# Performance work log

Measured on AMD Instinct MI355X. Metric: run time of the kernel, lower is better.

## Reference

```python
import jax, jax.numpy as jnp
import numpy as np

DIM = 256; HEADS = 8; HD = DIM // HEADS; WIN = 3; LOCAL = WIN * WIN
SR = 8; SHARED = 4; ROUTED = 2
B = 4; RES = 64; TBL = 4096
EPS = 1.1920929e-07  # torch.finfo(float32).eps


def _l2(x):
    return x / jnp.clip(jnp.linalg.norm(x, axis=-1, keepdims=True), EPS)


def _forward(x, relative_coords_table, q_w, q_b, kv_w, kv_b, temperature,
             query_embedding, rpb_local, learnable_tokens, learnable_bias,
             cpb1_w, cpb1_b, cpb2_w, cpb2_b, sr_w, sr_b, norm_g, norm_b,
             wg_w, wg0_w, wg1_w, proj_w, proj_b, relative_pos_index, H, W):
    B_, N, C = x.shape
    pH, pW = H // SR, W // SR
    PL = pH * pW
    _x = x.reshape(B_ * N, C)

    # ---- MoE head routing: top-k gating over routed heads ----
    gates = jax.nn.softmax(_x @ wg_w.T, axis=1)                 # (BN, n_routed)
    _, idx = jax.lax.top_k(gates, ROUTED)
    mask = jax.nn.one_hot(idx, gates.shape[1], dtype=gates.dtype).sum(axis=1)
    rg = gates * mask
    rg = rg / jnp.clip(jnp.sum(rg, axis=1, keepdims=True), EPS)
    routed_gates = rg.reshape(B_, N, -1) * ROUTED

    # ---- seq-length-scale buffer: log(local valid-window count + pool_len) ----
    r = WIN // 2
    ch = np.minimum(np.arange(H) + r, H - 1) - np.maximum(np.arange(H) - r, 0) + 1
    cw = np.minimum(np.arange(W) + r, W - 1) - np.maximum(np.arange(W) - r, 0) + 1
    sls = jnp.asarray(np.log(np.outer(ch, cw).reshape(-1, 1).astype(np.float32) + PL))

    # ---- queries ----
    q = (x @ q_w.T + q_b).reshape(B_, N, HEADS, HD).transpose(0, 2, 1, 3)
    q_norm = _l2(q)                                             # (B,h,N,d)
    q_scaled = (q_norm + query_embedding) * jax.nn.softplus(temperature) * sls

    # ---- local branch: unfold normalized k and v over 3x3 windows (zero pad) ----
    kv = x @ kv_w.T + kv_b                                      # (B,N,2C)
    k_loc = _l2(kv[..., :C].reshape(B_, N, HEADS, HD)).reshape(B_, N, C)
    kvl = jnp.concatenate([k_loc, kv[..., C:]], -1).transpose(0, 2, 1).reshape(B_, 2 * C, H, W)
    kvp = jnp.pad(kvl, ((0, 0), (0, 0), (r, r), (r, r)))
    patches = jnp.stack([kvp[:, :, i:i + H, j:j + W] for i in range(WIN) for j in range(WIN)], axis=2)
    patches = patches.reshape(B_, 2 * HEADS, HD, LOCAL, N).transpose(0, 1, 4, 2, 3)  # (B,2h,N,d,L)
    k_local, v_local = patches[:, :HEADS], patches[:, HEADS:]

    attn_local = jnp.einsum('bhnd,bhndl->bhnl', q_scaled, k_local) + rpb_local[:, None, :]

    # ---- pooled global branch ----
    x_ = x.transpose(0, 2, 1).reshape(B_, C, H, W)
    x_ = jnp.einsum('oc,bchw->bohw', sr_w, x_) + sr_b[None, :, None, None]  # 1x1 conv
    x_ = jax.nn.gelu(x_, approximate=False)
    x_ = x_.reshape(B_, C, pH, SR, pW, SR).mean((3, 5)).reshape(B_, C, PL).transpose(0, 2, 1)
    mu = x_.mean(-1, keepdims=True)
    var = ((x_ - mu) ** 2).mean(-1, keepdims=True)
    x_ = (x_ - mu) / jnp.sqrt(var + 1e-5) * norm_g + norm_b
    kvp2 = (x_ @ kv_w.T + kv_b).reshape(B_, PL, 2 * HEADS, HD).transpose(0, 2, 1, 3)
    k_pool, v_pool = kvp2[:, :HEADS], kvp2[:, HEADS:]

    cpb = jax.nn.relu(relative_coords_table @ cpb1_w.T + cpb1_b) @ cpb2_w.T + cpb2_b  # (T,h)
    pool_bias = cpb.T[:, relative_pos_index.reshape(-1)].reshape(HEADS, N, PL)
    attn_pool = jnp.einsum('bhnd,bhpd->bhnp', q_scaled, _l2(k_pool)) + pool_bias

    # ---- joint softmax over local + pooled keys ----
    attn = jax.nn.softmax(jnp.concatenate([attn_local, attn_pool], axis=-1), axis=-1)
    a_loc, a_pool = attn[..., :LOCAL], attn[..., LOCAL:]
    a_loc = jnp.einsum('bhnd,hdl->bhnl', q_norm, learnable_tokens) + learnable_bias + a_loc
    x_local = jnp.einsum('bhnl,bhndl->bhnd', a_loc, v_local)
    x_pool = jnp.einsum('bhnp,bhpd->bhnd', a_pool, v_pool)
    out = (x_local + x_pool).transpose(0, 2, 1, 3)              # (B,N,h,d)

    # ---- combine shared + routed head gates ----
    shared_gates = jax.nn.softmax(_x @ wg1_w.T, axis=1).reshape(B_, N, SHARED) * SHARED
    w0 = jax.nn.softmax(_x @ wg0_w.T, axis=1).reshape(B_, N, 2) * 2
    masked = jnp.concatenate([w0[..., 0:1] * shared_gates, w0[..., 1:2] * routed_gates], axis=-1)
    out = (masked[..., None] * out).reshape(B_, N, C)
    return out @ proj_w.T + proj_b


def setup_inputs() -> dict:
    key = jax.random.key(0)
    ks = jax.random.split(key, 20)
    H = W = RES
    N = H * W
    C = DIM
    PL = (H // SR) * (W // SR)

    def nrm(i, shape, s=0.02):
        return jax.random.normal(ks[i], shape, dtype=jnp.float32) * s

    return {
        'x': jax.random.normal(ks[0], (B, N, C), dtype=jnp.float32),
        'relative_coords_table': jax.random.normal(ks[1], (TBL, 2), dtype=jnp.float32),
        'q_w': nrm(3, (C, C)), 'q_b': jnp.zeros((C,), jnp.float32),
        'kv_w': nrm(4, (2 * C, C)), 'kv_b': jnp.zeros((2 * C,), jnp.float32),
        'temperature': jnp.full((HEADS, 1, 1), float(np.log(np.exp(1 / 0.24) - 1)), jnp.float32),
        'query_embedding': nrm(5, (HEADS, 1, HD)),
        'rpb_local': nrm(6, (HEADS, LOCAL), 0.0004),
        'learnable_tokens': nrm(7, (HEADS, HD, LOCAL)),
        'learnable_bias': jnp.zeros((HEADS, 1, LOCAL), jnp.float32),
        'cpb1_w': nrm(8, (512, 2)), 'cpb1_b': jnp.zeros((512,), jnp.float32),
        'cpb2_w': nrm(9, (HEADS, 512)), 'cpb2_b': jnp.zeros((HEADS,), jnp.float32),
        'sr_w': nrm(10, (C, C)), 'sr_b': jnp.zeros((C,), jnp.float32),
        'norm_g': jnp.ones((C,), jnp.float32), 'norm_b': jnp.zeros((C,), jnp.float32),
        'wg_w': nrm(11, (HEADS - SHARED, C)),
        'wg0_w': nrm(12, (2, C)),
        'wg1_w': nrm(13, (SHARED, C)),
        'proj_w': nrm(14, (C, C)), 'proj_b': jnp.zeros((C,), jnp.float32),
        'relative_pos_index': jax.random.randint(ks[2], (N, PL), 0, TBL, dtype=jnp.int32),
        'H': H, 'W': W,
    }


def reference(x, relative_coords_table, q_w, q_b, kv_w, kv_b, temperature,
              query_embedding, rpb_local, learnable_tokens, learnable_bias,
              cpb1_w, cpb1_b, cpb2_w, cpb2_b, sr_w, sr_b, norm_g, norm_b,
              wg_w, wg0_w, wg1_w, proj_w, proj_b, relative_pos_index, H, W):
    return _forward(x, relative_coords_table, q_w, q_b, kv_w, kv_b, temperature,
                    query_embedding, rpb_local, learnable_tokens, learnable_bias,
                    cpb1_w, cpb1_b, cpb2_w, cpb2_b, sr_w, sr_b, norm_g, norm_b,
                    wg_w, wg0_w, wg1_w, proj_w, proj_b, relative_pos_index, H, W)
```

## Files before the change

### kernel.cpp

```cpp
#include <hip/hip_runtime.h>
#include <math.h>

#define EPSF 1.1920929e-07f

typedef __attribute__((ext_vector_type(8))) short short8;
typedef __attribute__((ext_vector_type(4))) float f32x4;

static __device__ __forceinline__ unsigned short f2bf(float f) {
    unsigned int u = __float_as_uint(f);
    return (unsigned short)((u + 0x7FFFu + ((u >> 16) & 1u)) >> 16);
}
static __device__ __forceinline__ float bf2f(unsigned short u) {
    return __uint_as_float((unsigned int)u << 16);
}

__global__ __launch_bounds__(256) void prep_kernel(
    const float* __restrict__ x,
    const float* __restrict__ wg,  const float* __restrict__ wg0,
    const float* __restrict__ wg1,
    const float* __restrict__ q_w, const float* __restrict__ kv_w,
    const float* __restrict__ sr_w, const float* __restrict__ pw,
    const float* __restrict__ tbl,
    const float* __restrict__ c1w, const float* __restrict__ c1b,
    const float* __restrict__ c2w, const float* __restrict__ c2b,
    unsigned short* __restrict__ xbf, float* __restrict__ gate,
    unsigned short* __restrict__ wcat, unsigned short* __restrict__ pwbf,
    float* __restrict__ kv_wT, float* __restrict__ cpb)
{
    __shared__ float shpad[512];
    const int blk = blockIdx.x;
    const int t   = threadIdx.x;
    if (blk < 4096) {
        const int j = t & 63;
        const int row = (blk << 2) + (t >> 6);
        float4 v = *(const float4*)(x + (size_t)row*256 + j*4);
        ushort4 o;
        o.x = f2bf(v.x); o.y = f2bf(v.y); o.z = f2bf(v.z); o.w = f2bf(v.w);
        *(ushort4*)(xbf + (size_t)row*256 + j*4) = o;
        float d[10];
#pragma unroll
        for (int f = 0; f < 10; ++f) {
            const float* wf = (f < 4) ? (wg + f*256) : (f < 6) ? (wg0 + (f-4)*256)
                                                               : (wg1 + (f-6)*256);
            float4 wv = *(const float4*)(wf + j*4);
            float s = v.x*wv.x + v.y*wv.y + v.z*wv.z + v.w*wv.w;
            s += __shfl_xor(s, 32); s += __shfl_xor(s, 16); s += __shfl_xor(s, 8);
            s += __shfl_xor(s, 4);  s += __shfl_xor(s, 2);  s += __shfl_xor(s, 1);
            d[f] = s;
        }
        if (j == 0) {
            float e[4];
            float m = fmaxf(fmaxf(d[0],d[1]), fmaxf(d[2],d[3]));
            float ssum = 0.f;
            for (int i = 0; i < 4; ++i) { e[i] = expf(d[i]-m); ssum += e[i]; }
            for (int i = 0; i < 4; ++i) e[i] /= ssum;
            int i1 = 0;
            for (int i = 1; i < 4; ++i) if (e[i] > e[i1]) i1 = i;
            int i2 = -1;
            for (int i = 0; i < 4; ++i) if (i != i1 && (i2 < 0 || e[i] > e[i2])) i2 = i;
            float rs = fmaxf(e[i1] + e[i2], EPSF);
            float rg[4] = {0.f,0.f,0.f,0.f};
            rg[i1] = e[i1] / rs * 2.f;
            rg[i2] = e[i2] / rs * 2.f;
            float sh[4];
            float m1 = fmaxf(fmaxf(d[6],d[7]), fmaxf(d[8],d[9]));
            float s1 = 0.f;
            for (int i = 0; i < 4; ++i) { sh[i] = expf(d[6+i]-m1); s1 += sh[i]; }
            float mm = fmaxf(d[4], d[5]);
            float e0 = expf(d[4]-mm), e1 = expf(d[5]-mm);
            float w00 = e0/(e0+e1)*2.f, w01 = e1/(e0+e1)*2.f;
            float* gr = gate + ((size_t)row << 3);
            for (int i = 0; i < 4; ++i) gr[i]   = w00 * (sh[i]/s1*4.f);
            for (int i = 0; i < 4; ++i) gr[4+i] = w01 * rg[i];
        }
    } else if (blk < 4416) {
        const int e = ((blk - 4096)*256 + t)*4;
        if (e < 262144) {
            int n = e >> 8, k = e & 255;
            const float* src = (n < 256) ? (q_w + n*256) :
                               (n < 768) ? (kv_w + (n-256)*256) : (sr_w + (n-768)*256);
            float4 v = *(const float4*)(src + k);
            ushort4 o;
            o.x = f2bf(v.x); o.y = f2bf(v.y); o.z = f2bf(v.z); o.w = f2bf(v.w);
            *(ushort4*)(wcat + e) = o;
        } else {
            int e2 = e - 262144;
            float4 v = *(const float4*)(pw + e2);
            ushort4 o;
            o.x = f2bf(v.x); o.y = f2bf(v.y); o.z = f2bf(v.z); o.w = f2bf(v.w);
            *(ushort4*)(pwbf + e2) = o;
        }
    } else if (blk < 4544) {
        const int e = ((blk - 4416)*256 + t)*4;
        int o = e >> 8, k = e & 255;
        float4 v = *(const float4*)(kv_w + e);
        kv_wT[(k+0)*512 + o] = v.x;
        kv_wT[(k+1)*512 + o] = v.y;
        kv_wT[(k+2)*512 + o] = v.z;
        kv_wT[(k+3)*512 + o] = v.w;
    } else {
        const int r = blk - 4544;
        const float c0 = tbl[(size_t)r*2], c1 = tbl[(size_t)r*2+1];
        for (int i = t; i < 512; i += 256)
            shpad[i] = fmaxf(c0*c1w[i*2] + c1*c1w[i*2+1] + c1b[i], 0.f);
        __syncthreads();
        const int hh = t >> 5, dd = t & 31;
        float s = 0.f;
        for (int i = dd; i < 512; i += 32) s += shpad[i] * c2w[hh*512+i];
        for (int off = 16; off; off >>= 1) s += __shfl_xor(s, off, 32);
        if (dd == 0) cpb[((size_t)r << 3) + hh] = s + c2b[hh];
    }
}

__global__ __launch_bounds__(256) void gemm_mfma(
    const unsigned short* __restrict__ A,
    const unsigned short* __restrict__ W,
    const float* __restrict__ B0, const float* __restrict__ B1,
    const float* __restrict__ B2,
    int r1, int r2, int mode,
    float* __restrict__ C, int ldc,
    unsigned short* __restrict__ qkv,
    const float* __restrict__ temp, const float* __restrict__ qe)
{
    __shared__ __attribute__((aligned(16))) unsigned short Bt[64*264];
    const int m0 = blockIdx.y << 6;
    const int n0 = blockIdx.x << 6;
    const int t  = threadIdx.x;
    const int w  = t >> 6;
    const int col16 = t & 15;
    const int quad  = (t & 63) >> 4;

    const float* Bp; int noff;
    if (n0 < r1)      { Bp = B0; noff = 0;  }
    else if (n0 < r2) { Bp = B1; noff = r1; }
    else              { Bp = B2; noff = r2; }

    short8 afr[8];
    {
        const unsigned short* ap = A + (size_t)(m0 + w*16 + col16)*256 + quad*8;
#pragma unroll
        for (int kk = 0; kk < 8; ++kk)
            afr[kk] = *(const short8*)(ap + kk*32);
    }
#pragma unroll
    for (int j = 0; j < 8; ++j) {
        int ci = j*256 + t;
        int r = ci >> 5, c = ci & 31;
        uint4 bv = *(const uint4*)(W + (size_t)(n0 + r)*256 + c*8);
        *(uint4*)(Bt + r*264 + c*8) = bv;
    }
    __syncthreads();

    f32x4 acc[4];
#pragma unroll
    for (int ct = 0; ct < 4; ++ct) acc[ct] = (f32x4){0.f, 0.f, 0.f, 0.f};
#pragma unroll
    for (int kk = 0; kk < 8; ++kk) {
#pragma unroll
        for (int ct = 0; ct < 4; ++ct) {
            short8 bf = *(const short8*)(Bt + (ct*16 + col16)*264 + kk*32 + quad*8);
            acc[ct] = __builtin_amdgcn_mfma_f32_16x16x32_bf16(afr[kk], bf, acc[ct], 0, 0, 0);
        }
    }

    float bias_c[4];
#pragma unroll
    for (int ct = 0; ct < 4; ++ct)
        bias_c[ct] = Bp[n0 + ct*16 + col16 - noff];

    if (mode == 0) {
        const int region = n0 >> 8;
        float qe_c[4], spt_c[4];
        if (region == 0) {
#pragma unroll
            for (int c = 0; c < 4; ++c) {
                int col = n0 + c*16 + col16;
                spt_c[c] = log1pf(expf(temp[(col >> 5) & 7]));
                qe_c[c]  = qe[col];
            }
        }
#pragma unroll
        for (int reg = 0; reg < 4; ++reg) {
            const int row = m0 + w*16 + quad*4 + reg;
            float v[4];
#pragma unroll
            for (int c = 0; c < 4; ++c) v[c] = acc[c][reg] + bias_c[c];
            if (region <= 1) {
#pragma unroll
                for (int hp = 0; hp < 2; ++hp) {
                    float s = v[2*hp]*v[2*hp] + v[2*hp+1]*v[2*hp+1];
                    s += __shfl_xor(s, 1); s += __shfl_xor(s, 2);
                    s += __shfl_xor(s, 4); s += __shfl_xor(s, 8);
                    float inv = 1.0f / fmaxf(sqrtf(s), EPSF);
                    v[2*hp]   *= inv;
                    v[2*hp+1] *= inv;
                }
            }
            if (region == 0) {
                int n = row & 4095;
                int y = n >> 6, x = n & 63;
                int cy = (y == 0 || y == 63) ? 2 : 3;
                int cx = (x == 0 || x == 63) ? 2 : 3;
                float sls = logf((float)(cy*cx) + 64.0f);
#pragma unroll
                for (int c = 0; c < 4; ++c)
                    v[c] = (v[c] + qe_c[c]) * (spt_c[c] * sls);
            }
            if (region == 3) {
#pragma unroll
                for (int c = 0; c < 4; ++c) {
                    float g = 0.5f * v[c] * (1.0f + erff(v[c] * 0.70710678118654752f));
                    C[(size_t)row * ldc + n0 + c*16 + col16] = g;
                }
            } else {
#pragma unroll
                for (int c = 0; c < 4; ++c)
                    qkv[(size_t)row * 2048 + n0 + c*16 + col16] = f2bf(v[c]);
            }
        }
    } else {
#pragma unroll
        for (int reg = 0; reg < 4; ++reg) {
            const int row = m0 + w*16 + quad*4 + reg;
#pragma unroll
            for (int c = 0; c < 4; ++c)
                C[(size_t)row * ldc + n0 + c*16 + col16] = acc[c][reg] + bias_c[c];
        }
    }
}

__global__ __launch_bounds__(256) void poolkv_kernel(
    const float* __restrict__ buf,
    const float* __restrict__ g, const float* __restrict__ bb,
    const float* __restrict__ kv_wT, const float* __restrict__ kv_b,
    unsigned short* __restrict__ kpb, unsigned short* __restrict__ vpb)
{
    __shared__ float r1[256], r2[256];
    __shared__ float xs[256];
    __shared__ float rowv[512];
    __shared__ float inv[8];
    const int blk = blockIdx.x;
    const int b = blk >> 6, p = blk & 63;
    const int py = p >> 3, px = p & 7;
    const int t = threadIdx.x;
    float acc = 0.f;
    for (int dy = 0; dy < 8; ++dy)
#pragma unroll
        for (int dx = 0; dx < 8; ++dx) {
            int s = ((py*8+dy) << 6) + px*8 + dx;
            acc += buf[(((size_t)(b*4096+s)) << 10) + 768 + t];
        }
    acc *= (1.0f/64.0f);
    r1[t] = acc; r2[t] = acc*acc;
    __syncthreads();
    for (int off = 128; off; off >>= 1) {
        if (t < off) { r1[t] += r1[t+off]; r2[t] += r2[t+off]; }
        __syncthreads();
    }
    float mu  = r1[0] * (1.0f/256.0f);
    float var = r2[0] * (1.0f/256.0f) - mu*mu;
    float rstd = rsqrtf(var + 1e-5f);
    xs[t] = (acc - mu) * rstd * g[t] + bb[t];
    __syncthreads();
    {
        float s0 = kv_b[t], s1 = kv_b[256 + t];
#pragma unroll 4
        for (int k = 0; k < 256; ++k) {
            float xv = xs[k];
            const float* wr = kv_wT + (size_t)k*512;
            s0 += xv * wr[t];
            s1 += xv * wr[256 + t];
        }
        rowv[t] = s0; rowv[256 + t] = s1;
    }
    __syncthreads();
    if (t < 8) {
        float s = 0.f;
        for (int dd = 0; dd < 32; ++dd) { float v = rowv[t*32+dd]; s += v*v; }
        inv[t] = 1.0f / fmaxf(sqrtf(s), EPSF);
    }
    __syncthreads();
    const int h = t >> 5;
    size_t o = ((((size_t)(b*8+h))*64 + p) << 5) + (t & 31);
    kpb[o] = f2bf(rowv[t] * inv[h]);
    vpb[o] = f2bf(rowv[256 + t]);
}

__global__ __launch_bounds__(256, 4) void attn_mfma(
    const unsigned short* __restrict__ qkv,
    unsigned short* __restrict__ ao,
    const unsigned short* __restrict__ kpb,
    const unsigned short* __restrict__ vpb,
    const float* __restrict__ cpb,
    const int*   __restrict__ rpi,
    const float* __restrict__ temp,
    const float* __restrict__ qe,
    const float* __restrict__ rpb,
    const float* __restrict__ lt,
    const float* __restrict__ lb,
    const float* __restrict__ gate)
{
    __shared__ __attribute__((aligned(16))) unsigned short U0[112*40];
    __shared__ __attribute__((aligned(16))) unsigned short U1[64*40];
    __shared__ __attribute__((aligned(16))) unsigned short QS[64*40];
    __shared__ __attribute__((aligned(16))) unsigned short P[64*136];
    __shared__ __attribute__((aligned(16))) unsigned short LTT[16*40];
    __shared__ float invscL[64], gateL[64], rpbL[9], dqvL[16];
    __shared__ int hofs[112];

    const int tile = blockIdx.x;
    const int h    = blockIdx.y;
    const int b    = blockIdx.z;
    const int ty0  = (tile >> 3) << 3;
    const int tx0  = (tile & 7) << 3;
    const int t    = threadIdx.x;

    const float spt = log1pf(expf(temp[h]));
    if (t < 64) {
        int y = ty0 + (t >> 3), x = tx0 + (t & 7);
        int cy = (y == 0 || y == 63) ? 2 : 3;
        int cx = (x == 0 || x == 63) ? 2 : 3;
        invscL[t] = 1.0f / (spt * logf((float)(cy*cx) + 64.0f));
        gateL[t] = gate[(((size_t)(b*4096 + ((y<<6)|x))) << 3) + h];
    } else if (t < 80) {
        int j = t - 64;
        float s = 0.f;
        if (j < 9) {
            s = lb[h*9 + j];
            for (int dd = 0; dd < 32; ++dd)
                s -= qe[h*32+dd] * lt[(h*32+dd)*9 + j];
        }
        dqvL[j] = s;
    } else if (t < 89) {
        rpbL[t-80] = rpb[h*9 + (t-80)];
    } else if (t >= 128 && t < 240) {
        int r = t - 128;
        int off = -1;
        if (r < 100) {
            int y = ty0 + r/10 - 1, x = tx0 + r%10 - 1;
            if (y >= 0 && y < 64 && x >= 0 && x < 64)
                off = (b*4096 + ((y<<6)|x))*2048 + h*32;
        }
        hofs[r] = off;
    }
    for (int i = t; i < 16*32; i += 256) {
        int j = i >> 5, dd = i & 31;
        LTT[j*40 + dd] = (j < 9) ? f2bf(lt[(h*32+dd)*9 + j]) : (unsigned short)0;
    }
    __syncthreads();

    unsigned short* KH = U0;
    unsigned short* KP = U1;
    for (int i = t; i < 112*8; i += 256) {
        int r = i >> 3, sg = i & 7;
        int off = hofs[r];
        uint2 val = {0u, 0u};
        if (off >= 0)
            val = *(const uint2*)(qkv + (size_t)off + 256 + sg*4);
        *(uint2*)(KH + r*40 + sg*4) = val;
    }
    {
        const unsigned short* src = kpb + (size_t)(b*8+h)*2048;
        for (int i = t; i < 512; i += 256)
            *(uint2*)(KP + (i >> 3)*40 + (i & 7)*4) = *(const uint2*)(src + i*4);
    }
    for (int i = t; i < 512; i += 256) {
        int n = i >> 3, sg = i & 7;
        int off = hofs[(n >> 3)*10 + (n & 7) + 11];
        *(uint2*)(QS + n*40 + sg*4) = *(const uint2*)(qkv + (size_t)off + sg*4);
    }
    __syncthreads();

    const int lane  = t & 63;
    const int w     = t >> 6;
    const int col16 = lane & 15;
    const int quad  = lane >> 4;
    const int s_w   = (20*w) & ~15;

    float pbias[4][4];
#pragma unroll
    for (int ct = 0; ct < 4; ++ct) {
        int p = ct*16 + col16;
#pragma unroll
        for (int reg = 0; reg < 4; ++reg) {
            int n = w*16 + quad*4 + reg;
            int y = ty0 + (n >> 3), x = tx0 + (n & 7);
            int ngl = (y << 6) | x;
            pbias[ct][reg] = cpb[((size_t)rpi[(size_t)ngl*64 + p] << 3) + h];
        }
    }

    short8 aq = *(const short8*)(QS + (w*16 + col16)*40 + quad*8);
    f32x4 cl[4], cp[4];
    {
        const f32x4 z = {0.f, 0.f, 0.f, 0.f};
#pragma unroll
        for (int ct = 0; ct < 4; ++ct) {
            short8 bk = *(const short8*)(KH + (s_w + ct*16 + col16)*40 + quad*8);
            cl[ct] = __builtin_amdgcn_mfma_f32_16x16x32_bf16(aq, bk, z, 0, 0, 0);
        }
#pragma unroll
        for (int ct = 0; ct < 4; ++ct) {
            short8 bp = *(const short8*)(KP + (ct*16 + col16)*40 + quad*8);
            cp[ct] = __builtin_amdgcn_mfma_f32_16x16x32_bf16(aq, bp, z, 0, 0, 0);
        }
    }
#pragma unroll
    for (int ct = 0; ct < 4; ++ct) {
        int hk = s_w + ct*16 + col16;
        int ky = hk / 10, kx = hk - ky*10;
#pragma unroll
        for (int reg = 0; reg < 4; ++reg) {
            int n = w*16 + quad*4 + reg;
            int dy = ky - (n >> 3), dx = kx - (n & 7);
            bool valid = (dy >= 0 && dy <= 2 && dx >= 0 && dx <= 2);
            cl[ct][reg] = valid ? (cl[ct][reg] + rpbL[dy*3 + dx]) : -1e30f;
        }
    }
#pragma unroll
    for (int ct = 0; ct < 4; ++ct)
#pragma unroll
        for (int reg = 0; reg < 4; ++reg)
            cp[ct][reg] += pbias[ct][reg];
    float inv[4];
#pragma unroll
    for (int reg = 0; reg < 4; ++reg) {
        float m = -1e30f;
#pragma unroll
        for (int ct = 0; ct < 4; ++ct) m = fmaxf(m, cl[ct][reg]);
#pragma unroll
        for (int ct = 0; ct < 4; ++ct) m = fmaxf(m, cp[ct][reg]);
        m = fmaxf(m, __shfl_xor(m, 1)); m = fmaxf(m, __shfl_xor(m, 2));
        m = fmaxf(m, __shfl_xor(m, 4)); m = fmaxf(m, __shfl_xor(m, 8));
        float s = 0.f;
#pragma unroll
        for (int ct = 0; ct < 4; ++ct) {
            float e = __builtin_expf(cl[ct][reg] - m); cl[ct][reg] = e; s += e;
        }
#pragma unroll
        for (int ct = 0; ct < 4; ++ct) {
            float e = __builtin_expf(cp[ct][reg] - m); cp[ct][reg] = e; s += e;
        }
        s += __shfl_xor(s, 1); s += __shfl_xor(s, 2);
        s += __shfl_xor(s, 4); s += __shfl_xor(s, 8);
        inv[reg] = 1.0f / s;
    }
#pragma unroll
    for (int ct = 0; ct < 4; ++ct)
#pragma unroll
        for (int reg = 0; reg < 4; ++reg) {
            int n = w*16 + quad*4 + reg;
            P[n*136 + ct*16 + col16] = f2bf(cl[ct][reg] * inv[reg]);
        }
#pragma unroll
    for (int ct = 0; ct < 4; ++ct)
#pragma unroll
        for (int reg = 0; reg < 4; ++reg) {
            int n = w*16 + quad*4 + reg;
            P[n*136 + 64 + ct*16 + col16] = f2bf(cp[ct][reg] * inv[reg]);
        }
    {
        const f32x4 z = {0.f, 0.f, 0.f, 0.f};
        short8 blt = *(const short8*)(LTT + col16*40 + quad*8);
        f32x4 cd = __builtin_amdgcn_mfma_f32_16x16x32_bf16(aq, blt, z, 0, 0, 0);
        if (col16 < 9) {
            int dy = col16 / 3, dx = col16 - dy*3;
#pragma unroll
            for (int reg = 0; reg < 4; ++reg) {
                int n = w*16 + quad*4 + reg;
                float ltv = cd[reg] * invscL[n] + dqvL[col16];
                int hk = ((n >> 3) + dy)*10 + (n & 7) + dx;
                int pc = hk - s_w;
                P[n*136 + pc] = f2bf(bf2f(P[n*136 + pc]) + ltv);
            }
        }
    }
    __syncthreads();

    unsigned short* VT  = U0;
    unsigned short* VPT = U1;
    for (int i = t; i < 1792; i += 256) {
        int rlo = i & 15, rest = i >> 4;
        int dp = rest & 15, r = (rest >> 4)*16 + rlo;
        int off = hofs[r];
        unsigned val = 0;
        if (off >= 0)
            val = *(const unsigned*)(qkv + (size_t)off + 512 + dp*2);
        VT[(2*dp)*136 + r]   = (unsigned short)(val & 0xffffu);
        VT[(2*dp+1)*136 + r] = (unsigned short)(val >> 16);
    }
    for (int i = t; i < 1024; i += 256) {
        int plo = i & 15, rest = i >> 4;
        int dp = rest & 15, p = (rest >> 4)*16 + plo;
        unsigned val = *(const unsigned*)(vpb + (size_t)(b*8+h)*2048 + p*32 + dp*2);
        VPT[(2*dp)*72 + p]   = (unsigned short)(val & 0xffffu);
        VPT[(2*dp+1)*72 + p] = (unsigned short)(val >> 16);
    }
    __syncthreads();

    f32x4 o0 = {0.f,0.f,0.f,0.f}, o1 = {0.f,0.f,0.f,0.f};
#pragma unroll
    for (int ks = 0; ks < 4; ++ks) {
        short8 a = *(const short8*)(P + (w*16 + col16)*136 + ks*32 + quad*8);
        short8 b0, b1;
        if (ks < 2) {
            b0 = *(const short8*)(VT + col16*136      + s_w + ks*32 + quad*8);
            b1 = *(const short8*)(VT + (16+col16)*136 + s_w + ks*32 + quad*8);
        } else {
            b0 = *(const short8*)(VPT + col16*72      + (ks-2)*32 + quad*8);
            b1 = *(const short8*)(VPT + (16+col16)*72 + (ks-2)*32 + quad*8);
        }
        o0 = __builtin_amdgcn_mfma_f32_16x16x32_bf16(a, b0, o0, 0, 0, 0);
        o1 = __builtin_amdgcn_mfma_f32_16x16x32_bf16(a, b1, o1, 0, 0, 0);
    }
#pragma unroll
    for (int reg = 0; reg < 4; ++reg) {
        int n = w*16 + quad*4 + reg;
        int y = ty0 + (n >> 3), x = tx0 + (n & 7);
        size_t rowo = (size_t)(b*4096 + ((y<<6)|x))*256 + h*32;
        float g = gateL[n];
        ao[rowo + col16]      = f2bf(o0[reg] * g);
        ao[rowo + 16 + col16] = f2bf(o1[reg] * g);
    }
}

extern "C" void kernel_launch(void* const* d_in, const int* in_sizes, int n_in,
                              void* d_out, int out_size, void* d_ws, size_t ws_size,
                              hipStream_t stream)
{
    const float* x    = (const float*)d_in[0];
    const float* tbl  = (const float*)d_in[1];
    const float* q_w  = (const float*)d_in[2];
    const float* q_b  = (const float*)d_in[3];
    const float* kv_w = (const float*)d_in[4];
    const float* kv_b = (const float*)d_in[5];
    const float* temp = (const float*)d_in[6];
    const float* qe   = (const float*)d_in[7];
    const float* rpb  = (const float*)d_in[8];
    const float* lt   = (const float*)d_in[9];
    const float* lb   = (const float*)d_in[10];
    const float* c1w  = (const float*)d_in[11];
    const float* c1b  = (const float*)d_in[12];
    const float* c2w  = (const float*)d_in[13];
    const float* c2b  = (const float*)d_in[14];
    const float* sr_w = (const float*)d_in[15];
    const float* sr_b = (const float*)d_in[16];
    const float* ng   = (const float*)d_in[17];
    const float* nbias= (const float*)d_in[18];
    const float* wg   = (const float*)d_in[19];
    const float* wg0  = (const float*)d_in[20];
    const float* wg1  = (const float*)d_in[21];
    const float* pw   = (const float*)d_in[22];
    const float* pb   = (const float*)d_in[23];
    const int*   rpi  = (const int*)d_in[24];
    (void)in_sizes; (void)n_in; (void)out_size; (void)ws_size;

    float* buf   = (float*)d_ws;
    unsigned short* qkvb = (unsigned short*)d_ws;
    float* xp    = buf + (size_t)16384*1024;
    float* kpoolf= xp + 65536;
    unsigned short* kpb = (unsigned short*)kpoolf;
    unsigned short* vpb = kpb + 131072;
    float* cpbb  = kpoolf + 131072;
    float* gateb = cpbb + 32768;
    float* kvwT  = gateb + 131072;
    unsigned short* xbf  = (unsigned short*)(kvwT + 131072);
    unsigned short* ao   = xbf;
    unsigned short* wcat = xbf + (size_t)16384*256;
    unsigned short* pwbf = wcat + 262144;
    float* out   = (float*)d_out;

    prep_kernel<<<8640,256,0,stream>>>(x, wg, wg0, wg1, q_w, kv_w, sr_w, pw,
                                       tbl, c1w, c1b, c2w, c2b,
                                       xbf, gateb, wcat, pwbf, kvwT, cpbb);
    gemm_mfma<<<dim3(16,256),256,0,stream>>>(xbf, wcat, q_b, kv_b, sr_b,
                                             256, 768, 0, buf, 1024,
                                             qkvb, temp, qe);
    poolkv_kernel<<<256,256,0,stream>>>(buf, ng, nbias, kvwT, kv_b, kpb, vpb);
    attn_mfma<<<dim3(64,8,4),256,0,stream>>>(qkvb, ao, kpb, vpb, cpbb, rpi,
                                             temp, qe, rpb, lt, lb, gateb);
    gemm_mfma<<<dim3(4,256),256,0,stream>>>(ao, pwbf, pb, pb, pb,
                                            1<<30, 1<<30, 1, out, 256,
                                            (unsigned short*)nullptr, nullptr, nullptr);
}
```

Measured before the change: 248.4 us.

## Restructure attention kernel staging: per-head CPB table in LDS, exp2 softmax, pre-transposed V

The CPB bias table is stored head-major and pre-scaled by log2(e), then copied per block into shared memory so the gathered bias lookups hit LDS rather than global memory. Softmax moves to exp2 by folding log2(e) into temperature, relative bias and CPB. The pooled V is written pre-transposed by the producer, so the attention kernel can load it with vector copies. Shared memory is packed into one union buffer (reusing P for the CPB table, dropping QS, hofs and the per-row LDS arrays) to allow 5 blocks per CU, which adds an extra barrier and more register pressure.

```diff
diff --git a/kernel.cpp b/kernel.cpp
--- a/kernel.cpp
+++ b/kernel.cpp
@@ -108,7 +108,7 @@
         float s = 0.f;
         for (int i = dd; i < 512; i += 32) s += shpad[i] * c2w[hh*512+i];
         for (int off = 16; off; off >>= 1) s += __shfl_xor(s, off, 32);
-        if (dd == 0) cpb[((size_t)r << 3) + hh] = s + c2b[hh];
+        if (dd == 0) cpb[(size_t)hh*4096 + r] = (s + c2b[hh]) * 1.44269504089f;
     }
 }
 
@@ -175,7 +175,7 @@
 #pragma unroll
             for (int c = 0; c < 4; ++c) {
                 int col = n0 + c*16 + col16;
-                spt_c[c] = log1pf(expf(temp[(col >> 5) & 7]));
+                spt_c[c] = log1pf(expf(temp[(col >> 5) & 7])) * 1.44269504089f;
                 qe_c[c]  = qe[col];
             }
         }
@@ -280,13 +280,14 @@
         inv[t] = 1.0f / fmaxf(sqrtf(s), EPSF);
     }
     __syncthreads();
-    const int h = t >> 5;
-    size_t o = ((((size_t)(b*8+h))*64 + p) << 5) + (t & 31);
-    kpb[o] = f2bf(rowv[t] * inv[h]);
-    vpb[o] = f2bf(rowv[256 + t]);
+    const int h  = t >> 5;
+    const int dd = t & 31;
+    size_t ob = (size_t)(b*8+h) << 11;
+    kpb[ob + ((size_t)p << 5) + dd] = f2bf(rowv[t] * inv[h]);
+    vpb[ob + ((size_t)dd << 6) + p] = f2bf(rowv[256 + t]);
 }
 
-__global__ __launch_bounds__(256, 4) void attn_mfma(
+__global__ __launch_bounds__(256, 5) void attn_mfma(
     const unsigned short* __restrict__ qkv,
     unsigned short* __restrict__ ao,
     const unsigned short* __restrict__ kpb,
@@ -300,13 +301,14 @@
     const float* __restrict__ lb,
     const float* __restrict__ gate)
 {
-    __shared__ __attribute__((aligned(16))) unsigned short U0[112*40];
-    __shared__ __attribute__((aligned(16))) unsigned short U1[64*40];
-    __shared__ __attribute__((aligned(16))) unsigned short QS[64*40];
-    __shared__ __attribute__((aligned(16))) unsigned short P[64*136];
-    __shared__ __attribute__((aligned(16))) unsigned short LTT[16*40];
-    __shared__ float invscL[64], gateL[64], rpbL[9], dqvL[16];
-    __shared__ int hofs[112];
+    __shared__ __attribute__((aligned(16))) unsigned char SMEM[32624];
+    unsigned short* U0  = (unsigned short*)SMEM;
+    unsigned short* U1  = (unsigned short*)(SMEM + 8960);
+    unsigned short* P   = (unsigned short*)(SMEM + 14080);
+    unsigned short* LTT = (unsigned short*)(SMEM + 31488);
+    float* dqvL = (float*)(SMEM + 32512);
+    float* rpbL = (float*)(SMEM + 32576);
+    float* cpbL = (float*)P;
 
     const int tile = blockIdx.x;
     const int h    = blockIdx.y;
@@ -314,15 +316,48 @@
     const int ty0  = (tile >> 3) << 3;
     const int tx0  = (tile & 7) << 3;
     const int t    = threadIdx.x;
-
-    const float spt = log1pf(expf(temp[h]));
-    if (t < 64) {
-        int y = ty0 + (t >> 3), x = tx0 + (t & 7);
-        int cy = (y == 0 || y == 63) ? 2 : 3;
-        int cx = (x == 0 || x == 63) ? 2 : 3;
-        invscL[t] = 1.0f / (spt * logf((float)(cy*cx) + 64.0f));
-        gateL[t] = gate[(((size_t)(b*4096 + ((y<<6)|x))) << 3) + h];
-    } else if (t < 80) {
+    const int lane  = t & 63;
+    const int w     = t >> 6;
+    const int col16 = lane & 15;
+    const int quad  = lane >> 4;
+    const int s_w   = (20*w) & ~15;
+
+    const int nq = w*16 + col16;
+    const int qy = ty0 + (nq >> 3), qx = tx0 + (nq & 7);
+    short8 aq = *(const short8*)(qkv +
+        ((size_t)(b*4096 + ((qy<<6)|qx)))*2048 + h*32 + quad*8);
+
+    int rpv[4][4];
+#pragma unroll
+    for (int ct = 0; ct < 4; ++ct) {
+        int p = ct*16 + col16;
+#pragma unroll
+        for (int reg = 0; reg < 4; ++reg) {
+            int n = w*16 + quad*4 + reg;
+            int y = ty0 + (n >> 3), x = tx0 + (n & 7);
+            rpv[ct][reg] = rpi[(size_t)((y << 6) | x)*64 + p];
+        }
+    }
+
+    for (int i = t; i < 896; i += 256) {
+        int r = i >> 3, sg = i & 7;
+        uint2 val = {0u, 0u};
+        if (r < 100) {
+            int y = ty0 + r/10 - 1, x = tx0 + r%10 - 1;
+            if (y >= 0 && y < 64 && x >= 0 && x < 64)
+                val = *(const uint2*)(qkv +
+                    (size_t)(b*4096 + ((y<<6)|x))*2048 + h*32 + 256 + sg*4);
+        }
+        *(uint2*)(U0 + r*40 + sg*4) = val;
+    }
+    {
+        const unsigned short* src = kpb + (size_t)(b*8+h)*2048;
+        for (int i = t; i < 512; i += 256)
+            *(uint2*)(U1 + (i >> 3)*40 + (i & 7)*4) = *(const uint2*)(src + i*4);
+    }
+    const float spt  = log1pf(expf(temp[h]));
+    const float sptL = spt * 1.44269504089f;
+    if (t >= 64 && t < 80) {
         int j = t - 64;
         float s = 0.f;
         if (j < 9) {
@@ -331,77 +366,38 @@
                 s -= qe[h*32+dd] * lt[(h*32+dd)*9 + j];
         }
         dqvL[j] = s;
-    } else if (t < 89) {
-        rpbL[t-80] = rpb[h*9 + (t-80)];
-    } else if (t >= 128 && t < 240) {
-        int r = t - 128;
-        int off = -1;
-        if (r < 100) {
-            int y = ty0 + r/10 - 1, x = tx0 + r%10 - 1;
-            if (y >= 0 && y < 64 && x >= 0 && x < 64)
-                off = (b*4096 + ((y<<6)|x))*2048 + h*32;
-        }
-        hofs[r] = off;
-    }
-    for (int i = t; i < 16*32; i += 256) {
+    } else if (t >= 80 && t < 89) {
+        rpbL[t-80] = rpb[h*9 + (t-80)] * 1.44269504089f;
+    }
+    for (int i = t; i < 512; i += 256) {
         int j = i >> 5, dd = i & 31;
-        LTT[j*40 + dd] = (j < 9) ? f2bf(lt[(h*32+dd)*9 + j]) : (unsigned short)0;
-    }
-    __syncthreads();
-
-    unsigned short* KH = U0;
-    unsigned short* KP = U1;
-    for (int i = t; i < 112*8; i += 256) {
-        int r = i >> 3, sg = i & 7;
-        int off = hofs[r];
-        uint2 val = {0u, 0u};
-        if (off >= 0)
-            val = *(const uint2*)(qkv + (size_t)off + 256 + sg*4);
-        *(uint2*)(KH + r*40 + sg*4) = val;
+        LTT[j*32 + dd] = (j < 9) ? f2bf(lt[(h*32+dd)*9 + j]) : (unsigned short)0;
     }
     {
-        const unsigned short* src = kpb + (size_t)(b*8+h)*2048;
-        for (int i = t; i < 512; i += 256)
-            *(uint2*)(KP + (i >> 3)*40 + (i & 7)*4) = *(const uint2*)(src + i*4);
-    }
-    for (int i = t; i < 512; i += 256) {
-        int n = i >> 3, sg = i & 7;
-        int off = hofs[(n >> 3)*10 + (n & 7) + 11];
-        *(uint2*)(QS + n*40 + sg*4) = *(const uint2*)(qkv + (size_t)off + sg*4);
-    }
-    __syncthreads();
-
-    const int lane  = t & 63;
-    const int w     = t >> 6;
-    const int col16 = lane & 15;
-    const int quad  = lane >> 4;
-    const int s_w   = (20*w) & ~15;
+        const float4* src = (const float4*)(cpb + (size_t)h*4096);
+        float4* dst = (float4*)cpbL;
+        for (int i = t; i < 1024; i += 256) dst[i] = src[i];
+    }
+    __syncthreads();
 
     float pbias[4][4];
 #pragma unroll
-    for (int ct = 0; ct < 4; ++ct) {
-        int p = ct*16 + col16;
-#pragma unroll
-        for (int reg = 0; reg < 4; ++reg) {
-            int n = w*16 + quad*4 + reg;
-            int y = ty0 + (n >> 3), x = tx0 + (n & 7);
-            int ngl = (y << 6) | x;
-            pbias[ct][reg] = cpb[((size_t)rpi[(size_t)ngl*64 + p] << 3) + h];
-        }
-    }
-
-    short8 aq = *(const short8*)(QS + (w*16 + col16)*40 + quad*8);
+    for (int ct = 0; ct < 4; ++ct)
+#pragma unroll
+        for (int reg = 0; reg < 4; ++reg)
+            pbias[ct][reg] = cpbL[rpv[ct][reg]];
+
     f32x4 cl[4], cp[4];
     {
         const f32x4 z = {0.f, 0.f, 0.f, 0.f};
 #pragma unroll
         for (int ct = 0; ct < 4; ++ct) {
-            short8 bk = *(const short8*)(KH + (s_w + ct*16 + col16)*40 + quad*8);
+            short8 bk = *(const short8*)(U0 + (s_w + ct*16 + col16)*40 + quad*8);
             cl[ct] = __builtin_amdgcn_mfma_f32_16x16x32_bf16(aq, bk, z, 0, 0, 0);
         }
 #pragma unroll
         for (int ct = 0; ct < 4; ++ct) {
-            short8 bp = *(const short8*)(KP + (ct*16 + col16)*40 + quad*8);
+            short8 bp = *(const short8*)(U1 + (ct*16 + col16)*40 + quad*8);
             cp[ct] = __builtin_amdgcn_mfma_f32_16x16x32_bf16(aq, bp, z, 0, 0, 0);
         }
     }
@@ -422,6 +418,9 @@
 #pragma unroll
         for (int reg = 0; reg < 4; ++reg)
             cp[ct][reg] += pbias[ct][reg];
+
+    __syncthreads();
+
     float inv[4];
 #pragma unroll
     for (int reg = 0; reg < 4; ++reg) {
@@ -435,11 +434,11 @@
         float s = 0.f;
 #pragma unroll
         for (int ct = 0; ct < 4; ++ct) {
-            float e = __builtin_expf(cl[ct][reg] - m); cl[ct][reg] = e; s += e;
+            float e = exp2f(cl[ct][reg] - m); cl[ct][reg] = e; s += e;
         }
 #pragma unroll
         for (int ct = 0; ct < 4; ++ct) {
-            float e = __builtin_expf(cp[ct][reg] - m); cp[ct][reg] = e; s += e;
+            float e = exp2f(cp[ct][reg] - m); cp[ct][reg] = e; s += e;
         }
         s += __shfl_xor(s, 1); s += __shfl_xor(s, 2);
         s += __shfl_xor(s, 4); s += __shfl_xor(s, 8);
@@ -461,14 +460,20 @@
         }
     {
         const f32x4 z = {0.f, 0.f, 0.f, 0.f};
-        short8 blt = *(const short8*)(LTT + col16*40 + quad*8);
+        short8 blt = *(const short8*)(LTT + col16*32 + quad*8);
         f32x4 cd = __builtin_amdgcn_mfma_f32_16x16x32_bf16(aq, blt, z, 0, 0, 0);
         if (col16 < 9) {
+            const float iA = 1.0f / (sptL * 4.2195077052f);
+            const float iB = 1.0f / (sptL * 4.2484952420f);
+            const float iC = 1.0f / (sptL * 4.2904594411f);
             int dy = col16 / 3, dx = col16 - dy*3;
 #pragma unroll
             for (int reg = 0; reg < 4; ++reg) {
                 int n = w*16 + quad*4 + reg;
-                float ltv = cd[reg] * invscL[n] + dqvL[col16];
+                int y = ty0 + (n >> 3), x = tx0 + (n & 7);
+                int cs = ((y==0||y==63)?2:3) + ((x==0||x==63)?2:3);
+                float isc = (cs == 4) ? iA : (cs == 5) ? iB : iC;
+                float ltv = cd[reg] * isc + dqvL[col16];
                 int hk = ((n >> 3) + dy)*10 + (n & 7) + dx;
                 int pc = hk - s_w;
                 P[n*136 + pc] = f2bf(bf2f(P[n*136 + pc]) + ltv);
@@ -477,24 +482,36 @@
     }
     __syncthreads();
 
+    float gv[4];
+#pragma unroll
+    for (int reg = 0; reg < 4; ++reg) {
+        int n = w*16 + quad*4 + reg;
+        int y = ty0 + (n >> 3), x = tx0 + (n & 7);
+        gv[reg] = gate[(((size_t)(b*4096 + ((y<<6)|x))) << 3) + h];
+    }
     unsigned short* VT  = U0;
     unsigned short* VPT = U1;
-    for (int i = t; i < 1792; i += 256) {
-        int rlo = i & 15, rest = i >> 4;
-        int dp = rest & 15, r = (rest >> 4)*16 + rlo;
-        int off = hofs[r];
-        unsigned val = 0;
-        if (off >= 0)
-            val = *(const unsigned*)(qkv + (size_t)off + 512 + dp*2);
-        VT[(2*dp)*136 + r]   = (unsigned short)(val & 0xffffu);
-        VT[(2*dp+1)*136 + r] = (unsigned short)(val >> 16);
-    }
-    for (int i = t; i < 1024; i += 256) {
-        int plo = i & 15, rest = i >> 4;
-        int dp = rest & 15, p = (rest >> 4)*16 + plo;
-        unsigned val = *(const unsigned*)(vpb + (size_t)(b*8+h)*2048 + p*32 + dp*2);
-        VPT[(2*dp)*72 + p]   = (unsigned short)(val & 0xffffu);
-        VPT[(2*dp+1)*72 + p] = (unsigned short)(val >> 16);
+    for (int i = t; i < 896; i += 256) {
+        int r = i >> 3, sg = i & 7;
+        uint2 val = {0u, 0u};
+        if (r < 100) {
+            int y = ty0 + r/10 - 1, x = tx0 + r%10 - 1;
+            if (y >= 0 && y < 64 && x >= 0 && x < 64)
+                val = *(const uint2*)(qkv +
+                    (size_t)(b*4096 + ((y<<6)|x))*2048 + h*32 + 512 + sg*4);
+        }
+        int d0 = sg << 2;
+        VT[(d0+0)*136 + r] = (unsigned short)(val.x & 0xffffu);
+        VT[(d0+1)*136 + r] = (unsigned short)(val.x >> 16);
+        VT[(d0+2)*136 + r] = (unsigned short)(val.y & 0xffffu);
+        VT[(d0+3)*136 + r] = (unsigned short)(val.y >> 16);
+    }
+    {
+        const unsigned short* vsrc = vpb + (size_t)(b*8+h)*2048;
+        for (int i = t; i < 512; i += 256) {
+            int d = i >> 4, p4 = (i & 15) << 2;
+            *(uint2*)(VPT + d*72 + p4) = *(const uint2*)(vsrc + d*64 + p4);
+        }
     }
     __syncthreads();
 
@@ -518,7 +535,7 @@
         int n = w*16 + quad*4 + reg;
         int y = ty0 + (n >> 3), x = tx0 + (n & 7);
         size_t rowo = (size_t)(b*4096 + ((y<<6)|x))*256 + h*32;
-        float g = gateL[n];
+        float g = gv[reg];
         ao[rowo + col16]      = f2bf(o0[reg] * g);
         ao[rowo + 16 + col16] = f2bf(o1[reg] * g);
     }
```

After: 225.4 us. -9.2%, faster.
